# Optimization experiments

Hardware: AMD Instinct MI355X
Metric: run time of the kernel (lower is better)

The kernel has to match this reference:

```python
import jax, jax.numpy as jnp
import numpy as np

APN, UEN, H, S = 105, 4000, 128, 10
BN_EPS = 1e-5


def _xavier(k, shape):
    fan_out, fan_in = shape
    return jax.random.normal(k, shape, dtype=jnp.float32) * jnp.sqrt(2.0 / (fan_in + fan_out))


def setup_inputs() -> dict:
    key = jax.random.key(0)
    ks = jax.random.split(key, 24)
    inp = {
        "pl": jax.random.normal(ks[0], (APN, UEN), dtype=jnp.float32),
        "require": jax.random.normal(ks[1], (UEN,), dtype=jnp.float32),
        "adj_ue": jax.random.randint(ks[2], (UEN, S), 0, APN, dtype=jnp.int32),
        "adj_ap": jax.random.randint(ks[3], (APN, S), 0, UEN, dtype=jnp.int32),
        # layer-1 Mean_layer weights [embed_dim, feature_dim]
        "W1_ap1": _xavier(ks[4], (H, UEN + APN)),
        "W1_ap2": _xavier(ks[5], (H, 2 * UEN)),
        "W1_ue1": _xavier(ks[6], (H, UEN + APN)),
        "W1_ue2": _xavier(ks[7], (H, 2 * APN)),
        # layer-2 Mean_layer weights
        "W2_ap1": _xavier(ks[8], (H, 4 * H)),
        "W2_ap2": _xavier(ks[9], (H, 4 * H)),
        "W2_ue1": _xavier(ks[10], (H, 4 * H)),
        "W2_ue2": _xavier(ks[11], (H, 4 * H)),
        # heads
        "weight_ap1": _xavier(ks[12], (2 * H, 2 * H)),
        "weight_ap2": _xavier(ks[13], (1, 2 * H)),
        "bais_ap": jax.random.uniform(ks[14], (APN,), dtype=jnp.float32),
        "weight_ue": _xavier(ks[15], (APN, 2 * H)),
        "bais_ue": jax.random.uniform(ks[16], (UEN,), dtype=jnp.float32),
        # BatchNorm1d affine params (training mode, batch stats)
        "bn_gamma": jnp.ones((2 * H,), dtype=jnp.float32),
        "bn_beta": jnp.zeros((2 * H,), dtype=jnp.float32),
    }
    return inp


def _agg(feats, idx):
    # GraphSage mean aggregate, exactly mask.sum/(num_neigh+1) of the original
    g = jnp.take(feats, idx, axis=0)            # [N, S, F]
    return g.sum(axis=1) / (idx.shape[1] + 1.0)  # [N, F]


def _two_hop(one_adj, sec_adj):
    # deterministic stand-in for union(sec_adj over one-hop) + sample(num_sample)
    s = one_adj.shape[1]
    g = jnp.take(sec_adj, one_adj, axis=0)       # [N, S, S]
    d = jnp.arange(s)
    return g[:, d, d]                            # [N, S]


def _layer(W, self_f, other_f, idx):
    comb = jnp.concatenate([self_f, _agg(other_f, idx)], axis=1)  # [N, feat]
    return jax.nn.relu(W @ comb.T)               # [H, N]


def _forward(pl, require, adj_ue, adj_ap, W1_ap1, W1_ap2, W1_ue1, W1_ue2,
             W2_ap1, W2_ap2, W2_ue1, W2_ue2, weight_ap1, weight_ap2,
             bais_ap, weight_ue, bais_ue, bn_gamma, bn_beta):
    feats_ap = pl            # [APN, UEN]
    feats_ue = pl.T          # [UEN, APN]

    ap2ap = _two_hop(adj_ap, adj_ue)   # AP -> AP 2-hop [APN, S]
    ue2ue = _two_hop(adj_ue, adj_ap)   # UE -> UE 2-hop [UEN, S]

    x1 = _layer(W1_ap1, feats_ap, feats_ue, adj_ap)   # [H, APN]
    x2 = _layer(W1_ap2, feats_ap, feats_ap, ap2ap)    # [H, APN]
    x3 = _layer(W1_ue1, feats_ue, feats_ap, adj_ue)   # [H, UEN]
    x4 = _layer(W1_ue2, feats_ue, feats_ue, ue2ue)    # [H, UEN]

    X_ap = jnp.concatenate([x1, x2], axis=0).T        # [APN, 2H]
    X_ue = jnp.concatenate([x3, x4], axis=0).T        # [UEN, 2H]

    x5 = _layer(W2_ap1, X_ap, X_ue, adj_ap)
    x6 = _layer(W2_ap2, X_ap, X_ap, ap2ap)
    x7 = _layer(W2_ue1, X_ue, X_ap, adj_ue)
    x8 = _layer(W2_ue2, X_ue, X_ue, ue2ue)

    X_ap2 = jnp.concatenate([x5, x6], axis=0)         # [2H, APN]
    hidden_pc = weight_ap1 @ X_ap2 + bais_ap          # [2H, APN] + [APN]
    PCoutcome = jax.nn.sigmoid((weight_ap2 @ hidden_pc).T)  # [APN, 1]

    X_ue2 = jnp.concatenate([x7, x8], axis=0)         # [2H, UEN]
    xt = X_ue2.T                                      # [UEN, 2H]
    mean = xt.mean(axis=0)
    var = xt.var(axis=0)                              # biased, training-mode BN
    xbn = ((xt - mean) / jnp.sqrt(var + BN_EPS)) * bn_gamma + bn_beta
    UA = weight_ue @ xbn.T + bais_ue                  # [APN, UEN] + [UEN]

    UA_ori = UA.T                                     # [UEN, APN]
    mx = UA_ori.max(axis=1, keepdims=True)
    mn = UA_ori.min(axis=1, keepdims=True)
    nor = (UA_ori - mx) / (mx - mn)
    UA_de = jax.nn.softmax(nor * 1000.0, axis=1)
    UA_st = jax.nn.softmax(nor, axis=1)
    var_ue = jnp.var(weight_ue, axis=1, ddof=1)       # torch.var unbiased
    return (UA_ori, UA_de, UA_st, PCoutcome, jnp.sum(var_ue))


def reference(pl, require, adj_ue, adj_ap, W1_ap1, W1_ap2, W1_ue1, W1_ue2,
              W2_ap1, W2_ap2, W2_ue1, W2_ue2, weight_ap1, weight_ap2,
              bais_ap, weight_ue, bais_ue, bn_gamma, bn_beta):
    return _forward(pl, require, adj_ue, adj_ap, W1_ap1, W1_ap2, W1_ue1,
                    W1_ue2, W2_ap1, W2_ap2, W2_ue1, W2_ue2, weight_ap1,
                    weight_ap2, bais_ap, weight_ue, bais_ue, bn_gamma, bn_beta)
```

## Files before the change

kernel.cpp:

```cpp
#include <hip/hip_runtime.h>
#include <math.h>
#include <float.h>


#define APN 105
#define UEN 4000
#define H   128
#define H2  256
#define SS  10
#define INV_NEIGH (1.0f/11.0f)
#define NKS 16
#define KSL 250

__device__ __forceinline__ float frelu(float v){ return v > 0.f ? v : 0.f; }

__global__ void k_twohop(const int* __restrict__ adj_ue, const int* __restrict__ adj_ap,
                         int* __restrict__ ap2ap, int* __restrict__ ue2ue){
  int idx = blockIdx.x*256 + threadIdx.x;
  if (idx >= (APN+UEN)*SS) return;
  if (idx < APN*SS){
    int s = idx % SS;
    ap2ap[idx] = adj_ue[adj_ap[idx]*SS + s];
  } else {
    int j = idx - APN*SS;
    int s = j % SS;
    ue2ue[j] = adj_ap[adj_ue[j]*SS + s];
  }
}

__device__ __forceinline__ void tile_core(const float (*As)[68], const float (*Bs)[68],
                                          int tx, int ty, float acc[4][4])
{
  #pragma unroll 4
  for (int k=0;k<32;k++){
    float a0 = As[k][ty*4+0], a1 = As[k][ty*4+1];
    float a2 = As[k][ty*4+2], a3 = As[k][ty*4+3];
    float b0 = Bs[k][tx*4+0], b1 = Bs[k][tx*4+1];
    float b2 = Bs[k][tx*4+2], b3 = Bs[k][tx*4+3];
    acc[0][0]=fmaf(a0,b0,acc[0][0]); acc[0][1]=fmaf(a0,b1,acc[0][1]);
    acc[0][2]=fmaf(a0,b2,acc[0][2]); acc[0][3]=fmaf(a0,b3,acc[0][3]);
    acc[1][0]=fmaf(a1,b0,acc[1][0]); acc[1][1]=fmaf(a1,b1,acc[1][1]);
    acc[1][2]=fmaf(a1,b2,acc[1][2]); acc[1][3]=fmaf(a1,b3,acc[1][3]);
    acc[2][0]=fmaf(a2,b0,acc[2][0]); acc[2][1]=fmaf(a2,b1,acc[2][1]);
    acc[2][2]=fmaf(a2,b2,acc[2][2]); acc[2][3]=fmaf(a2,b3,acc[2][3]);
    acc[3][0]=fmaf(a3,b0,acc[3][0]); acc[3][1]=fmaf(a3,b1,acc[3][1]);
    acc[3][2]=fmaf(a3,b2,acc[3][2]); acc[3][3]=fmaf(a3,b3,acc[3][3]);
  }
}

__global__ __launch_bounds__(256) void k_gemA6(
    const float* __restrict__ pl, const float* __restrict__ W1ap1,
    const float* __restrict__ W1ap2, const float* __restrict__ W1ue1,
    float* __restrict__ partial)
{
  __shared__ float As[32][68], Bs[32][68];
  int t = threadIdx.x;
  int n0 = blockIdx.x*64;
  int y = blockIdx.y;
  int ks = blockIdx.z;
  int slice = y>>1, h0 = (y&1)*64, k0 = ks*KSL;
  const float* w; int lda;
  if      (slice == 0){ w = W1ap1;       lda = UEN+APN; }
  else if (slice == 1){ w = W1ap2;       lda = 2*UEN;   }
  else if (slice == 2){ w = W1ap2 + UEN; lda = 2*UEN;   }
  else                { w = W1ue1 + APN; lda = UEN+APN; }
  int tx = t&15, ty = t>>4;
  int hr = t>>2, c0 = (t&3)*8;
  float acc[4][4] = {};
  for (int kc = 0; kc < 256; kc += 32){
    float w8[8], x8[8];
    const float* wr = w + (size_t)(h0+hr)*lda + k0 + kc + c0;
    #pragma unroll
    for (int i=0;i<8;i++) w8[i] = (kc+c0+i < KSL) ? wr[i] : 0.f;
    const float* xr = pl + (size_t)(n0+hr)*UEN + k0 + kc + c0;
    bool nok = (n0+hr < APN);
    #pragma unroll
    for (int i=0;i<8;i++) x8[i] = (nok && kc+c0+i < KSL) ? xr[i] : 0.f;
    __syncthreads();
    #pragma unroll
    for (int i=0;i<8;i++) As[c0+i][hr] = w8[i];
    #pragma unroll
    for (int i=0;i<8;i++) Bs[c0+i][hr] = x8[i];
    __syncthreads();
    tile_core(As, Bs, tx, ty, acc);
  }
  float* po = partial + (size_t)(slice*NKS+ks)*APN*H;
  #pragma unroll
  for (int j=0;j<4;j++){
    int n = n0 + tx*4 + j;
    if (n < APN){
      #pragma unroll
      for (int i=0;i<4;i++) po[(size_t)n*H + h0 + ty*4 + i] = acc[i][j];
    }
  }
}

__global__ __launch_bounds__(256) void k_redA(const float* __restrict__ partial,
                                              float* __restrict__ RA){
  int idx = blockIdx.x*256 + threadIdx.x;
  if (idx >= 4*APN*H) return;
  int slice = idx / (APN*H), r = idx % (APN*H);
  float s = 0.f;
  #pragma unroll
  for (int ks=0;ks<NKS;ks++) s += partial[((size_t)(slice*NKS+ks)*APN*H) + r];
  RA[idx] = s;
}

__global__ __launch_bounds__(256) void k_gemB2(
    const float* __restrict__ pl, const float* __restrict__ W1ap1,
    const float* __restrict__ W1ue1, const float* __restrict__ W1ue2,
    float* __restrict__ T3, float* __restrict__ T4,
    float* __restrict__ U1, float* __restrict__ R4)
{
  __shared__ float As[32][68], Bs[32][68];
  int t = threadIdx.x, u0 = blockIdx.x*64, y = blockIdx.y;
  int z = y>>1, h0 = (y&1)*64;
  const float* w; int lda; float* op;
  if      (z == 0){ w = W1ue1;       lda = UEN+APN; op = T3; }
  else if (z == 1){ w = W1ue2;       lda = 2*APN;   op = T4; }
  else if (z == 2){ w = W1ap1 + UEN; lda = UEN+APN; op = U1; }
  else            { w = W1ue2 + APN; lda = 2*APN;   op = R4; }
  int tx = t&15, ty = t>>4;
  int hr = t>>2,  c0 = (t&3)*8;
  int kr = t>>3, uu0 = (t&7)*8;
  float acc[4][4] = {};
  for (int kc=0; kc<128; kc+=32){
    float w8[8], x8[8];
    const float* wr = w + (size_t)(h0+hr)*lda + kc + c0;
    #pragma unroll
    for (int i=0;i<8;i++) w8[i] = (kc+c0+i < APN) ? wr[i] : 0.f;
    const float* xr = pl + (size_t)(kc+kr)*UEN + u0 + uu0;
    #pragma unroll
    for (int i=0;i<8;i++)
      x8[i] = (kc+kr < APN && u0+uu0+i < UEN) ? xr[i] : 0.f;
    __syncthreads();
    #pragma unroll
    for (int i=0;i<8;i++) As[c0+i][hr] = w8[i];
    #pragma unroll
    for (int i=0;i<8;i++) Bs[kr][uu0+i] = x8[i];
    __syncthreads();
    tile_core(As, Bs, tx, ty, acc);
  }
  #pragma unroll
  for (int j=0;j<4;j++){
    int u = u0 + tx*4 + j;
    if (u < UEN){
      #pragma unroll
      for (int i=0;i<4;i++) op[(size_t)u*H + h0 + ty*4 + i] = acc[i][j];
    }
  }
}

__global__ __launch_bounds__(256) void k_gemC2(
    const float* __restrict__ Xue, const float* __restrict__ W2ue1,
    const float* __restrict__ W2ue2, float* __restrict__ X2ue,
    float* __restrict__ Yb8)
{
  __shared__ float As[32][68], Bs[32][68];
  int t = threadIdx.x, u0 = blockIdx.x*64, y = blockIdx.y;
  int z = y>>1, h0 = (y&1)*64;
  const float* W = (z == 0) ? W2ue1 : W2ue2;
  int coff = (z == 2) ? H2 : 0;
  float* op; int ldo;
  if      (z == 0){ op = X2ue + h0;     ldo = H2; }
  else if (z == 1){ op = X2ue + H + h0; ldo = H2; }
  else            { op = Yb8 + h0;      ldo = H;  }
  int tx = t&15, ty = t>>4;
  int hr = t>>2, c0 = (t&3)*8;
  float acc[4][4] = {};
  for (int kc=0; kc<H2; kc+=32){
    float w8[8], x8[8];
    const float* wr = W + (size_t)(h0+hr)*(2*H2) + coff + kc + c0;
    #pragma unroll
    for (int i=0;i<8;i++) w8[i] = wr[i];
    const float* xr = Xue + (size_t)(u0+hr)*H2 + kc + c0;
    bool uok = (u0+hr < UEN);
    #pragma unroll
    for (int i=0;i<8;i++) x8[i] = uok ? xr[i] : 0.f;
    __syncthreads();
    #pragma unroll
    for (int i=0;i<8;i++) As[c0+i][hr] = w8[i];
    #pragma unroll
    for (int i=0;i<8;i++) Bs[c0+i][hr] = x8[i];
    __syncthreads();
    tile_core(As, Bs, tx, ty, acc);
  }
  #pragma unroll
  for (int j=0;j<4;j++){
    int u = u0 + tx*4 + j;
    if (u < UEN){
      #pragma unroll
      for (int i=0;i<4;i++) op[(size_t)u*ldo + ty*4 + i] = acc[i][j];
    }
  }
}

__global__ __launch_bounds__(256) void k_x_ueB(
    const float* __restrict__ T3, const float* __restrict__ T4,
    const float* __restrict__ P3t, const float* __restrict__ R4,
    const int* __restrict__ adj_ue, const int* __restrict__ ue2ue,
    float* __restrict__ Xue)
{
  __shared__ int aj[SS], u2[SS];
  int u = blockIdx.x, t = threadIdx.x;
  if (t < SS){ aj[t] = adj_ue[u*SS+t]; u2[t] = ue2ue[u*SS+t]; }
  __syncthreads();
  int h = t & (H-1);
  float g, s = 0.f;
  if (t < H){
    g = T3[(size_t)u*H + h];
    for (int q=0;q<SS;q++) s += P3t[(size_t)aj[q]*H + h];
  } else {
    g = T4[(size_t)u*H + h];
    for (int q=0;q<SS;q++) s += R4[(size_t)u2[q]*H + h];
  }
  Xue[(size_t)u*H2 + t] = frelu(g + s*INV_NEIGH);
}

__global__ __launch_bounds__(256) void k_x_ap(
    const float* __restrict__ RA, const float* __restrict__ U1,
    const int* __restrict__ adj_ap, const int* __restrict__ ap2ap,
    float* __restrict__ Xap)
{
  __shared__ int aj[SS], a2[SS];
  int i = blockIdx.x, t = threadIdx.x;
  if (t < SS){ aj[t] = adj_ap[i*SS+t]; a2[t] = ap2ap[i*SS+t]; }
  __syncthreads();
  int h = t & (H-1);
  float g, s = 0.f;
  if (t < H){
    g = RA[(size_t)i*H + h];
    for (int q=0;q<SS;q++) s += U1[(size_t)aj[q]*H + h];
  } else {
    g = RA[(size_t)APN*H + (size_t)i*H + h];
    const float* Q2t = RA + (size_t)2*APN*H;
    for (int q=0;q<SS;q++) s += Q2t[(size_t)a2[q]*H + h];
  }
  Xap[(size_t)i*H2 + t] = frelu(g + s*INV_NEIGH);
}

__global__ __launch_bounds__(128) void k_p7(
    const float* __restrict__ Xap, const float* __restrict__ W2ue1,
    float* __restrict__ P7t)
{
  __shared__ float xrow[H2];
  int n = blockIdx.x, t = threadIdx.x;
  xrow[t] = Xap[(size_t)n*H2 + t];
  xrow[t+128] = Xap[(size_t)n*H2 + t + 128];
  __syncthreads();
  const float* w = W2ue1 + (size_t)t*(2*H2) + H2;
  float s0=0.f,s1=0.f,s2=0.f,s3=0.f;
  for (int c=0;c<H2;c+=4){
    s0 = fmaf(w[c  ], xrow[c  ], s0);
    s1 = fmaf(w[c+1], xrow[c+1], s1);
    s2 = fmaf(w[c+2], xrow[c+2], s2);
    s3 = fmaf(w[c+3], xrow[c+3], s3);
  }
  P7t[(size_t)n*H + t] = (s0+s1)+(s2+s3);
}

__global__ __launch_bounds__(256) void k_x7x8b(
    float* __restrict__ X2ue, const float* __restrict__ P7t,
    const float* __restrict__ Yb8, const int* __restrict__ adj_ue,
    const int* __restrict__ ue2ue)
{
  __shared__ int aj[SS], u2[SS];
  int u = blockIdx.x, t = threadIdx.x;
  if (t < SS){ aj[t] = adj_ue[u*SS+t]; u2[t] = ue2ue[u*SS+t]; }
  __syncthreads();
  float g = X2ue[(size_t)u*H2 + t];
  float s = 0.f;
  if (t < H){
    for (int q=0;q<SS;q++) s += P7t[(size_t)aj[q]*H + t];
  } else {
    for (int q=0;q<SS;q++) s += Yb8[(size_t)u2[q]*H + (t-H)];
  }
  X2ue[(size_t)u*H2 + t] = frelu(g + s*INV_NEIGH);
}

__global__ __launch_bounds__(256) void k_ap_layer2_head(
    const float* __restrict__ Xap, const float* __restrict__ Xue,
    const float* __restrict__ W2ap1, const float* __restrict__ W2ap2,
    const int* __restrict__ adj_ap, const int* __restrict__ ap2ap,
    const float* __restrict__ wap1, const float* __restrict__ wap2,
    const float* __restrict__ bais_ap, float* __restrict__ out_pc)
{
  __shared__ float xa[H2], a5[H2], a6[H2], xs2[H2], red[256];
  __shared__ int aj[SS], a2i[SS];
  int i = blockIdx.x, t = threadIdx.x;
  if (t < SS){ aj[t] = adj_ap[i*SS+t]; a2i[t] = ap2ap[i*SS+t]; }
  __syncthreads();
  xa[t] = Xap[(size_t)i*H2+t];
  float s5=0.f, s6=0.f;
  for (int q=0;q<SS;q++){
    s5 += Xue[(size_t)aj[q]*H2 + t];
    s6 += Xap[(size_t)a2i[q]*H2 + t];
  }
  a5[t]=s5*INV_NEIGH; a6[t]=s6*INV_NEIGH;
  __syncthreads();
  const float* w; const float* agg;
  if (t < H){ w = W2ap1 + (size_t)t*(2*H2);     agg = a5; }
  else      { w = W2ap2 + (size_t)(t-H)*(2*H2); agg = a6; }
  float s0=0.f,s1=0.f,s2=0.f,s3=0.f;
  for (int c=0;c<H2;c+=4){
    s0 = fmaf(w[c  ], xa[c  ], s0);
    s1 = fmaf(w[c+1], xa[c+1], s1);
    s2 = fmaf(w[c+2], xa[c+2], s2);
    s3 = fmaf(w[c+3], xa[c+3], s3);
  }
  for (int c=0;c<H2;c+=4){
    s0 = fmaf(w[H2+c  ], agg[c  ], s0);
    s1 = fmaf(w[H2+c+1], agg[c+1], s1);
    s2 = fmaf(w[H2+c+2], agg[c+2], s2);
    s3 = fmaf(w[H2+c+3], agg[c+3], s3);
  }
  xs2[t] = frelu((s0+s1)+(s2+s3));
  __syncthreads();
  float hid = bais_ap[i];
  const float* wr1 = wap1 + (size_t)t*H2;
  for (int c=0;c<H2;c++) hid = fmaf(wr1[c], xs2[c], hid);
  red[t] = wap2[t]*hid;
  __syncthreads();
  for (int o=128;o>0;o>>=1){ if (t<o) red[t]+=red[t+o]; __syncthreads(); }
  if (t==0) out_pc[i] = 1.f/(1.f+expf(-red[0]));
}

__global__ __launch_bounds__(256) void k_bn_part(const float* __restrict__ X2ue,
                                                 float* __restrict__ part){
  int b = blockIdx.x, c = threadIdx.x;
  float s=0.f, s2=0.f;
  for (int u = b*125; u < (b+1)*125; u++){
    float v = X2ue[(size_t)u*H2 + c];
    s += v; s2 += v*v;
  }
  part[b*512 + c] = s;
  part[b*512 + 256 + c] = s2;
}

__global__ __launch_bounds__(256) void k_bn_final(
    const float* __restrict__ part, const float* __restrict__ gamma,
    const float* __restrict__ beta, const float* __restrict__ wue,
    float* __restrict__ scsh, float* __restrict__ out_scalar)
{
  __shared__ float red[256];
  int t = threadIdx.x;
  float s=0.f, s2=0.f;
  for (int b=0;b<32;b++){ s += part[b*512+t]; s2 += part[b*512+256+t]; }
  float mean = s*(1.f/UEN);
  float var  = s2*(1.f/UEN) - mean*mean;
  float sc = gamma[t]*rsqrtf(var + 1e-5f);
  scsh[t]    = sc;
  scsh[H2+t] = beta[t] - mean*sc;
  float vsum = 0.f;
  if (t < APN){
    const float* wr = wue + (size_t)t*H2;
    float S=0.f, S2=0.f;
    for (int c=0;c<H2;c++){ float w=wr[c]; S+=w; S2+=w*w; }
    vsum = (S2 - S*S*(1.f/H2)) * (1.f/(H2-1));
  }
  red[t]=vsum; __syncthreads();
  for (int o=128;o>0;o>>=1){ if (t<o) red[t]+=red[t+o]; __syncthreads(); }
  if (t==0) out_scalar[0]=red[0];
}

__global__ __launch_bounds__(128) void k_ua_head(
    const float* __restrict__ X2ue, const float* __restrict__ scsh,
    const float* __restrict__ wue, const float* __restrict__ bais_ue,
    float* __restrict__ out)
{
  __shared__ float xs[4][H2];
  __shared__ float rmax[128], rmin[128], rs1[128], rs2[128];
  int u0 = blockIdx.x*4, t = threadIdx.x;
  #pragma unroll
  for (int q=0;q<4;q++){
    xs[q][t]     = X2ue[(size_t)(u0+q)*H2 + t]*scsh[t] + scsh[H2+t];
    xs[q][t+128] = X2ue[(size_t)(u0+q)*H2 + t + 128]*scsh[t+128] + scsh[H2+t+128];
  }
  __syncthreads();
  int a = t;
  float acc[4] = {0.f,0.f,0.f,0.f};
  if (a < APN){
    const float* wr = wue + (size_t)a*H2;
    for (int c=0;c<H2;c++){
      float w = wr[c];
      acc[0] = fmaf(w, xs[0][c], acc[0]);
      acc[1] = fmaf(w, xs[1][c], acc[1]);
      acc[2] = fmaf(w, xs[2][c], acc[2]);
      acc[3] = fmaf(w, xs[3][c], acc[3]);
    }
    #pragma unroll
    for (int q=0;q<4;q++) acc[q] += bais_ue[u0+q];
  }
  for (int q=0;q<4;q++){
    rmax[t] = (a<APN) ? acc[q] : -FLT_MAX;
    rmin[t] = (a<APN) ? acc[q] :  FLT_MAX;
    __syncthreads();
    for (int o=64;o>0;o>>=1){
      if (t<o){ rmax[t]=fmaxf(rmax[t],rmax[t+o]); rmin[t]=fminf(rmin[t],rmin[t+o]); }
      __syncthreads();
    }
    float mx = rmax[0], mn = rmin[0];
    __syncthreads();
    float nor = (a<APN) ? (acc[q]-mx)/(mx-mn) : 0.f;
    float e1 = (a<APN) ? expf(nor*1000.f) : 0.f;
    float e2 = (a<APN) ? expf(nor)        : 0.f;
    rs1[t]=e1; rs2[t]=e2;
    __syncthreads();
    for (int o=64;o>0;o>>=1){
      if (t<o){ rs1[t]+=rs1[t+o]; rs2[t]+=rs2[t+o]; }
      __syncthreads();
    }
    float s1=rs1[0], s2=rs2[0];
    __syncthreads();
    if (a<APN){
      size_t u = u0+q;
      out[u*APN + a]                     = acc[q];
      out[(size_t)UEN*APN   + u*APN + a] = e1/s1;
      out[(size_t)2*UEN*APN + u*APN + a] = e2/s2;
    }
  }
}

extern "C" void kernel_launch(void* const* d_in, const int* in_sizes, int n_in,
                              void* d_out, int out_size, void* d_ws, size_t ws_size,
                              hipStream_t stream) {
  const float* pl      = (const float*)d_in[0];
  const int*   adj_ue  = (const int*)d_in[2];
  const int*   adj_ap  = (const int*)d_in[3];
  const float* W1ap1   = (const float*)d_in[4];
  const float* W1ap2   = (const float*)d_in[5];
  const float* W1ue1   = (const float*)d_in[6];
  const float* W1ue2   = (const float*)d_in[7];
  const float* W2ap1   = (const float*)d_in[8];
  const float* W2ap2   = (const float*)d_in[9];
  const float* W2ue1   = (const float*)d_in[10];
  const float* W2ue2   = (const float*)d_in[11];
  const float* wap1    = (const float*)d_in[12];
  const float* wap2    = (const float*)d_in[13];
  const float* bais_ap = (const float*)d_in[14];
  const float* wue     = (const float*)d_in[15];
  const float* bais_ue = (const float*)d_in[16];
  const float* gamma   = (const float*)d_in[17];
  const float* beta    = (const float*)d_in[18];
  float* out = (float*)d_out;
  (void)in_sizes; (void)n_in; (void)out_size; (void)ws_size;

  char* ws = (char*)d_ws;
  size_t off = 0;
  auto alloc = [&](size_t bytes)->char*{
    char* p = ws + off; off += (bytes + 255) & ~(size_t)255; return p;
  };
  int*   ap2ap = (int*)alloc(APN*SS*4);
  int*   ue2ue = (int*)alloc(UEN*SS*4);
  float* Xap   = (float*)alloc((size_t)APN*H2*4);
  float* Xue   = (float*)alloc((size_t)UEN*H2*4);
  float* X2ue  = (float*)alloc((size_t)UEN*H2*4);
  float* part  = (float*)alloc(32*512*4);
  float* scsh  = (float*)alloc(2*H2*4);
  float* partialA = Xue;
  float* T3 = X2ue;
  float* T4 = X2ue + 512000;
  float* U1  = out;
  float* Yb8 = out;
  float* R4  = out + 520000;
  float* RA  = out + 1040000;
  float* P3t = RA + (size_t)3*APN*H;
  float* P7t = out + 1100000;

  k_twohop        <<<dim3(((APN+UEN)*SS+255)/256), 256, 0, stream>>>(adj_ue, adj_ap, ap2ap, ue2ue);
  k_gemA6         <<<dim3(2,8,NKS), 256, 0, stream>>>(pl, W1ap1, W1ap2, W1ue1, partialA);
  k_redA          <<<dim3((4*APN*H+255)/256), 256, 0, stream>>>(partialA, RA);
  k_gemB2         <<<dim3((UEN+63)/64, 8), 256, 0, stream>>>(pl, W1ap1, W1ue1, W1ue2,
                                                             T3, T4, U1, R4);
  k_x_ueB         <<<dim3(UEN), 256, 0, stream>>>(T3, T4, P3t, R4, adj_ue, ue2ue, Xue);
  k_x_ap          <<<dim3(APN), 256, 0, stream>>>(RA, U1, adj_ap, ap2ap, Xap);
  k_p7            <<<dim3(APN), 128, 0, stream>>>(Xap, W2ue1, P7t);
  k_gemC2         <<<dim3((UEN+63)/64, 6), 256, 0, stream>>>(Xue, W2ue1, W2ue2, X2ue, Yb8);
  k_ap_layer2_head<<<dim3(APN), 256, 0, stream>>>(Xap, Xue, W2ap1, W2ap2, adj_ap, ap2ap,
                                                  wap1, wap2, bais_ap,
                                                  out + (size_t)3*UEN*APN);
  k_x7x8b         <<<dim3(UEN), 256, 0, stream>>>(X2ue, P7t, Yb8, adj_ue, ue2ue);
  k_bn_part       <<<dim3(32), 256, 0, stream>>>(X2ue, part);
  k_bn_final      <<<dim3(1), 256, 0, stream>>>(part, gamma, beta, wue, scsh,
                                                out + (size_t)3*UEN*APN + APN);
  k_ua_head       <<<dim3(UEN/4), 128, 0, stream>>>(X2ue, scsh, wue, bais_ue, out);
}
```

Before: 269.8 us.

## Fold BN scale into transposed head weights and use wave-shuffle reductions

BatchNorm's scale is folded into a transposed copy of the UE head weights, and its shift into a per-row offset computed once in the final BN kernel, so the head kernel reads raw activations. The head now handles 8 users per block with coalesced weight loads, and replaces its shared-memory tree reductions with wave shuffles plus a two-entry combine. The BN partial-sum kernel also uses more blocks. The single-block finalize kernel takes on extra work writing the 105x256 transposed weights, and the larger accumulator array adds register pressure.

```diff
diff --git a/kernel.cpp b/kernel.cpp
--- a/kernel.cpp
+++ b/kernel.cpp
@@ -11,6 +11,7 @@
 #define INV_NEIGH (1.0f/11.0f)
 #define NKS 16
 #define KSL 250
+#define BNB 80
 
 __device__ __forceinline__ float frelu(float v){ return v > 0.f ? v : 0.f; }
 
@@ -329,7 +330,7 @@
                                                  float* __restrict__ part){
   int b = blockIdx.x, c = threadIdx.x;
   float s=0.f, s2=0.f;
-  for (int u = b*125; u < (b+1)*125; u++){
+  for (int u = b*50; u < (b+1)*50; u++){
     float v = X2ue[(size_t)u*H2 + c];
     s += v; s2 += v*v;
   }
@@ -337,25 +338,33 @@
   part[b*512 + 256 + c] = s2;
 }
 
-__global__ __launch_bounds__(256) void k_bn_final(
+__global__ __launch_bounds__(256) void k_bn_final2(
     const float* __restrict__ part, const float* __restrict__ gamma,
     const float* __restrict__ beta, const float* __restrict__ wue,
-    float* __restrict__ scsh, float* __restrict__ out_scalar)
-{
-  __shared__ float red[256];
+    float* __restrict__ Wue_st, float* __restrict__ row_off,
+    float* __restrict__ out_scalar)
+{
+  __shared__ float shs[H2], red[256];
   int t = threadIdx.x;
   float s=0.f, s2=0.f;
-  for (int b=0;b<32;b++){ s += part[b*512+t]; s2 += part[b*512+256+t]; }
+  for (int b=0;b<BNB;b++){ s += part[b*512+t]; s2 += part[b*512+256+t]; }
   float mean = s*(1.f/UEN);
   float var  = s2*(1.f/UEN) - mean*mean;
   float sc = gamma[t]*rsqrtf(var + 1e-5f);
-  scsh[t]    = sc;
-  scsh[H2+t] = beta[t] - mean*sc;
+  shs[t] = beta[t] - mean*sc;
+  for (int a=0;a<APN;a++)
+    Wue_st[(size_t)t*APN + a] = wue[(size_t)a*H2 + t]*sc;
+  __syncthreads();
   float vsum = 0.f;
   if (t < APN){
     const float* wr = wue + (size_t)t*H2;
-    float S=0.f, S2=0.f;
-    for (int c=0;c<H2;c++){ float w=wr[c]; S+=w; S2+=w*w; }
+    float ro=0.f, S=0.f, S2=0.f;
+    for (int c=0;c<H2;c++){
+      float w = wr[c];
+      ro = fmaf(w, shs[c], ro);
+      S += w; S2 += w*w;
+    }
+    row_off[t] = ro;
     vsum = (S2 - S*S*(1.f/H2)) * (1.f/(H2-1));
   }
   red[t]=vsum; __syncthreads();
@@ -363,60 +372,64 @@
   if (t==0) out_scalar[0]=red[0];
 }
 
-__global__ __launch_bounds__(128) void k_ua_head(
-    const float* __restrict__ X2ue, const float* __restrict__ scsh,
-    const float* __restrict__ wue, const float* __restrict__ bais_ue,
+__global__ __launch_bounds__(128) void k_ua_head2(
+    const float* __restrict__ X2ue, const float* __restrict__ Wue_st,
+    const float* __restrict__ row_off, const float* __restrict__ bais_ue,
     float* __restrict__ out)
 {
-  __shared__ float xs[4][H2];
-  __shared__ float rmax[128], rmin[128], rs1[128], rs2[128];
-  int u0 = blockIdx.x*4, t = threadIdx.x;
+  __shared__ float xs[8][H2];
+  __shared__ float wmax[2], wmin[2], ws1[2], ws2[2];
+  int u0 = blockIdx.x*8, t = threadIdx.x;
   #pragma unroll
-  for (int q=0;q<4;q++){
-    xs[q][t]     = X2ue[(size_t)(u0+q)*H2 + t]*scsh[t] + scsh[H2+t];
-    xs[q][t+128] = X2ue[(size_t)(u0+q)*H2 + t + 128]*scsh[t+128] + scsh[H2+t+128];
+  for (int q=0;q<8;q++){
+    xs[q][t]     = X2ue[(size_t)(u0+q)*H2 + t];
+    xs[q][t+128] = X2ue[(size_t)(u0+q)*H2 + t + 128];
   }
   __syncthreads();
   int a = t;
-  float acc[4] = {0.f,0.f,0.f,0.f};
+  float acc[8];
+  #pragma unroll
+  for (int q=0;q<8;q++) acc[q] = 0.f;
   if (a < APN){
-    const float* wr = wue + (size_t)a*H2;
+    float ro = row_off[a];
+    #pragma unroll
+    for (int q=0;q<8;q++) acc[q] = ro + bais_ue[u0+q];
     for (int c=0;c<H2;c++){
-      float w = wr[c];
-      acc[0] = fmaf(w, xs[0][c], acc[0]);
-      acc[1] = fmaf(w, xs[1][c], acc[1]);
-      acc[2] = fmaf(w, xs[2][c], acc[2]);
-      acc[3] = fmaf(w, xs[3][c], acc[3]);
-    }
-    #pragma unroll
-    for (int q=0;q<4;q++) acc[q] += bais_ue[u0+q];
-  }
-  for (int q=0;q<4;q++){
-    rmax[t] = (a<APN) ? acc[q] : -FLT_MAX;
-    rmin[t] = (a<APN) ? acc[q] :  FLT_MAX;
-    __syncthreads();
-    for (int o=64;o>0;o>>=1){
-      if (t<o){ rmax[t]=fmaxf(rmax[t],rmax[t+o]); rmin[t]=fminf(rmin[t],rmin[t+o]); }
-      __syncthreads();
-    }
-    float mx = rmax[0], mn = rmin[0];
-    __syncthreads();
+      float w = Wue_st[(size_t)c*APN + a];
+      #pragma unroll
+      for (int q=0;q<8;q++) acc[q] = fmaf(w, xs[q][c], acc[q]);
+    }
+  }
+  int wid = t>>6;
+  for (int q=0;q<8;q++){
+    float vmax = (a<APN) ? acc[q] : -FLT_MAX;
+    float vmin = (a<APN) ? acc[q] :  FLT_MAX;
+    #pragma unroll
+    for (int o=32;o>0;o>>=1){
+      vmax = fmaxf(vmax, __shfl_xor(vmax, o));
+      vmin = fminf(vmin, __shfl_xor(vmin, o));
+    }
+    if ((t&63)==0){ wmax[wid]=vmax; wmin[wid]=vmin; }
+    __syncthreads();
+    float mx = fmaxf(wmax[0], wmax[1]);
+    float mn = fminf(wmin[0], wmin[1]);
     float nor = (a<APN) ? (acc[q]-mx)/(mx-mn) : 0.f;
     float e1 = (a<APN) ? expf(nor*1000.f) : 0.f;
     float e2 = (a<APN) ? expf(nor)        : 0.f;
-    rs1[t]=e1; rs2[t]=e2;
-    __syncthreads();
-    for (int o=64;o>0;o>>=1){
-      if (t<o){ rs1[t]+=rs1[t+o]; rs2[t]+=rs2[t+o]; }
-      __syncthreads();
-    }
-    float s1=rs1[0], s2=rs2[0];
-    __syncthreads();
-    if (a<APN){
+    float s1 = e1, s2 = e2;
+    #pragma unroll
+    for (int o=32;o>0;o>>=1){
+      s1 += __shfl_xor(s1, o);
+      s2 += __shfl_xor(s2, o);
+    }
+    if ((t&63)==0){ ws1[wid]=s1; ws2[wid]=s2; }
+    __syncthreads();
+    float S1 = ws1[0]+ws1[1], S2 = ws2[0]+ws2[1];
+    if (a < APN){
       size_t u = u0+q;
       out[u*APN + a]                     = acc[q];
-      out[(size_t)UEN*APN   + u*APN + a] = e1/s1;
-      out[(size_t)2*UEN*APN + u*APN + a] = e2/s2;
+      out[(size_t)UEN*APN   + u*APN + a] = e1/S1;
+      out[(size_t)2*UEN*APN + u*APN + a] = e2/S2;
     }
   }
 }
@@ -450,13 +463,14 @@
   auto alloc = [&](size_t bytes)->char*{
     char* p = ws + off; off += (bytes + 255) & ~(size_t)255; return p;
   };
-  int*   ap2ap = (int*)alloc(APN*SS*4);
-  int*   ue2ue = (int*)alloc(UEN*SS*4);
-  float* Xap   = (float*)alloc((size_t)APN*H2*4);
-  float* Xue   = (float*)alloc((size_t)UEN*H2*4);
-  float* X2ue  = (float*)alloc((size_t)UEN*H2*4);
-  float* part  = (float*)alloc(32*512*4);
-  float* scsh  = (float*)alloc(2*H2*4);
+  int*   ap2ap  = (int*)alloc(APN*SS*4);
+  int*   ue2ue  = (int*)alloc(UEN*SS*4);
+  float* Xap    = (float*)alloc((size_t)APN*H2*4);
+  float* Xue    = (float*)alloc((size_t)UEN*H2*4);
+  float* X2ue   = (float*)alloc((size_t)UEN*H2*4);
+  float* part   = (float*)alloc((size_t)BNB*512*4);
+  float* Wue_st = (float*)alloc((size_t)H2*APN*4);
+  float* rowoff = (float*)alloc(APN*4);
   float* partialA = Xue;
   float* T3 = X2ue;
   float* T4 = X2ue + 512000;
@@ -480,8 +494,8 @@
                                                   wap1, wap2, bais_ap,
                                                   out + (size_t)3*UEN*APN);
   k_x7x8b         <<<dim3(UEN), 256, 0, stream>>>(X2ue, P7t, Yb8, adj_ue, ue2ue);
-  k_bn_part       <<<dim3(32), 256, 0, stream>>>(X2ue, part);
-  k_bn_final      <<<dim3(1), 256, 0, stream>>>(part, gamma, beta, wue, scsh,
+  k_bn_part       <<<dim3(BNB), 256, 0, stream>>>(X2ue, part);
+  k_bn_final2     <<<dim3(1), 256, 0, stream>>>(part, gamma, beta, wue, Wue_st, rowoff,
                                                 out + (size_t)3*UEN*APN + APN);
-  k_ua_head       <<<dim3(UEN/4), 128, 0, stream>>>(X2ue, scsh, wue, bais_ue, out);
-}
+  k_ua_head2      <<<dim3(UEN/8), 128, 0, stream>>>(X2ue, Wue_st, rowoff, bais_ue, out);
+}
```

New measurement: 268.5 us. Within noise of the previous version (-0.5%).
